# Performance work log

Hardware: AMD Instinct MI355X
Metric: run time of the kernel (lower is better)

## Reference

```python
import jax, jax.numpy as jnp
import numpy as np

B, S, D, H = 1, 2048, 768, 12
WIN = 128            # window_size
HALF = WIN // 2      # 64
WN = WIN + 1         # each position attends to [i-64, i+64] inclusive -> 129 keys
DH = D // H


def setup_inputs() -> dict:
    key = jax.random.key(0)
    ks = jax.random.split(key, 8)
    scale = 0.02
    return {
        "query": jax.random.normal(ks[0], (B, S, D), dtype=jnp.float32),
        "key":   jax.random.normal(ks[1], (B, S, D), dtype=jnp.float32),
        "value": jax.random.normal(ks[2], (B, S, D), dtype=jnp.float32),
        "Wq": jax.random.normal(ks[3], (D, D), dtype=jnp.float32) * scale,
        "bq": jnp.zeros((D,), dtype=jnp.float32),
        "Wk": jax.random.normal(ks[4], (D, D), dtype=jnp.float32) * scale,
        "bk": jnp.zeros((D,), dtype=jnp.float32),
        "Wv": jax.random.normal(ks[5], (D, D), dtype=jnp.float32) * scale,
        "bv": jnp.zeros((D,), dtype=jnp.float32),
        "Wo": jax.random.normal(ks[6], (D, D), dtype=jnp.float32) * scale,
        "bo": jnp.zeros((D,), dtype=jnp.float32),
    }


def reference(query, key, value, Wq, bq, Wk, bk, Wv, bv, Wo, bo):
    b, s, d = query.shape
    # Linear projections, split heads: [B,S,H,DH]
    q = (query @ Wq + bq).reshape(b, s, H, DH)
    k = (key   @ Wk + bk).reshape(b, s, H, DH)
    v = (value @ Wv + bv).reshape(b, s, H, DH)

    # Window gather indices: pos[i, j] = i - HALF + j, j in [0, WN)
    pos = jnp.arange(s)[:, None] + (jnp.arange(WN)[None, :] - HALF)  # [S, WN]
    valid = (pos >= 0) & (pos < s)                                   # [S, WN]
    idx = jnp.clip(pos, 0, s - 1)

    kw = k[:, idx]  # [B, S, WN, H, DH]
    vw = v[:, idx]  # [B, S, WN, H, DH]

    scores = jnp.einsum('bshd,bswhd->bhsw', q, kw) / np.sqrt(DH)     # [B,H,S,WN]
    scores = jnp.where(valid[None, None, :, :], scores, -jnp.inf)
    attn = jax.nn.softmax(scores, axis=-1)

    ctx = jnp.einsum('bhsw,bswhd->bshd', attn, vw).reshape(b, s, d)  # [B,S,D]
    return ctx @ Wo + bo
```

## Files before the change

### kernel.cpp

```cpp
#include <hip/hip_runtime.h>
#include <math.h>

#define S_LEN 2048
#define DM 768
#define NHEAD 12
#define DHEAD 64
#define HALF_W 64

typedef _Float16 half8 __attribute__((ext_vector_type(8)));
typedef _Float16 half4_t __attribute__((ext_vector_type(4)));
typedef float floatx4 __attribute__((ext_vector_type(4)));

typedef const __attribute__((address_space(1))) unsigned int* gas_ptr;
typedef __attribute__((address_space(3))) unsigned int* las_ptr;
__device__ __forceinline__ void gld_lds16(const void* g, void* l) {
  __builtin_amdgcn_global_load_lds((gas_ptr)g, (las_ptr)l, 16, 0, 0);
}

__global__ __launch_bounds__(256)
void prep_kernel(const float* __restrict__ Wq, const float* __restrict__ Wk,
                 const float* __restrict__ Wv, const float* __restrict__ Wo,
                 _Float16* __restrict__ Tq, _Float16* __restrict__ Tk,
                 _Float16* __restrict__ Tv, _Float16* __restrict__ To,
                 const float* __restrict__ qs, const float* __restrict__ ks,
                 const float* __restrict__ vs, _Float16* __restrict__ Aq,
                 _Float16* __restrict__ Ak, _Float16* __restrict__ Av) {
  __shared__ float t[64][65];
  int b = blockIdx.x;
  if (b < 576) {
    int z = b / 144, rem = b % 144;
    const float* W = z == 0 ? Wq : z == 1 ? Wk : z == 2 ? Wv : Wo;
    _Float16* T = z == 0 ? Tq : z == 1 ? Tk : z == 2 ? Tv : To;
    int n0 = (rem % 12) * 64, k0 = (rem / 12) * 64;
    int tx = threadIdx.x & 15, ty = threadIdx.x >> 4;
#pragma unroll
    for (int i = 0; i < 4; ++i) {
      int row = ty + i * 16;
      float4 v = *(const float4*)(W + (size_t)(k0 + row) * DM + n0 + tx * 4);
      t[row][tx * 4 + 0] = v.x; t[row][tx * 4 + 1] = v.y;
      t[row][tx * 4 + 2] = v.z; t[row][tx * 4 + 3] = v.w;
    }
    __syncthreads();
#pragma unroll
    for (int i = 0; i < 4; ++i) {
      int nn = ty + i * 16, kk = tx * 4;
      half4_t h = {(_Float16)t[kk + 0][nn], (_Float16)t[kk + 1][nn],
                   (_Float16)t[kk + 2][nn], (_Float16)t[kk + 3][nn]};
      *(half4_t*)(T + (size_t)(n0 + nn) * DM + k0 + kk) = h;
    }
  } else {
    int i = b - 576;
    int z = i / 1536;
    const float* s = z == 0 ? qs : z == 1 ? ks : vs;
    _Float16* d = z == 0 ? Aq : z == 1 ? Ak : Av;
    int idx = (i % 1536) * 256 + threadIdx.x;
    float4 v = ((const float4*)s)[idx];
    half4_t h = {(_Float16)v.x, (_Float16)v.y, (_Float16)v.z, (_Float16)v.w};
    ((half4_t*)d)[idx] = h;
  }
}

#define GBM 128
#define GBN 128
#define GBK 64

__global__ __launch_bounds__(256, 2)
void gemm_f16_kernel(const _Float16* __restrict__ A0, const _Float16* __restrict__ A1,
                     const _Float16* __restrict__ A2, const _Float16* __restrict__ W0,
                     const _Float16* __restrict__ W1, const _Float16* __restrict__ W2,
                     const float* __restrict__ b0, const float* __restrict__ b1,
                     const float* __restrict__ b2, _Float16* __restrict__ H0,
                     _Float16* __restrict__ H1, _Float16* __restrict__ Vt,
                     float* __restrict__ Cf, int fp32_out) {
  __shared__ __align__(16) _Float16 As[GBM * GBK];
  __shared__ __align__(16) _Float16 Bs[GBN * GBK];
  const int z = blockIdx.z;
  const _Float16* A = z == 0 ? A0 : z == 1 ? A1 : A2;
  const _Float16* Wt = z == 0 ? W0 : z == 1 ? W1 : W2;
  const float* bias = z == 0 ? b0 : z == 1 ? b1 : b2;

  const int tid = threadIdx.x;
  const int lane = tid & 63;
  const int w = tid >> 6;
  const int lr = lane & 15;
  const int lq = lane >> 4;
  const int wm = w >> 1, wn = w & 1;
  const int m0 = blockIdx.y * GBM;
  const int n0 = blockIdx.x * GBN;
  const int wb = tid & 192;

  floatx4 acc[4][4] = {};

  for (int k0 = 0; k0 < DM; k0 += GBK) {
    __syncthreads();
#pragma unroll
    for (int i = 0; i < 4; ++i) {
      int c = i * 256 + tid;
      int m = c >> 3, j = c & 7;
      int jg = j ^ (m & 7);
      gld_lds16(A + (size_t)(m0 + m) * DM + k0 + jg * 8, &As[(i * 256 + wb) * 8]);
    }
#pragma unroll
    for (int i = 0; i < 4; ++i) {
      int c = i * 256 + tid;
      int n = c >> 3, j = c & 7;
      int jg = j ^ (n & 7);
      gld_lds16(Wt + (size_t)(n0 + n) * DM + k0 + jg * 8, &Bs[(i * 256 + wb) * 8]);
    }
    __syncthreads();

#pragma unroll
    for (int kh = 0; kh < 2; ++kh) {
      half8 af[4], bf[4];
#pragma unroll
      for (int mt = 0; mt < 4; ++mt) {
        int m = wm * 64 + mt * 16 + lr;
        int j = (kh * 4 + lq) ^ (m & 7);
        af[mt] = *(const half8*)&As[m * GBK + j * 8];
      }
#pragma unroll
      for (int nt = 0; nt < 4; ++nt) {
        int n = wn * 64 + nt * 16 + lr;
        int j = (kh * 4 + lq) ^ (n & 7);
        bf[nt] = *(const half8*)&Bs[n * GBK + j * 8];
      }
#pragma unroll
      for (int mt = 0; mt < 4; ++mt)
#pragma unroll
        for (int nt = 0; nt < 4; ++nt)
          acc[mt][nt] = __builtin_amdgcn_mfma_f32_16x16x32_f16(af[mt], bf[nt], acc[mt][nt], 0, 0, 0);
    }
  }

#pragma unroll
  for (int mt = 0; mt < 4; ++mt) {
    int row0 = m0 + wm * 64 + mt * 16 + lq * 4;
#pragma unroll
    for (int nt = 0; nt < 4; ++nt) {
      int col = n0 + wn * 64 + nt * 16 + lr;
      float bv = bias[col];
      if (fp32_out) {
#pragma unroll
        for (int rr = 0; rr < 4; ++rr)
          Cf[(size_t)(row0 + rr) * DM + col] = acc[mt][nt][rr] + bv;
      } else if (z == 2) {
        half4_t o = {(_Float16)(acc[mt][nt][0] + bv), (_Float16)(acc[mt][nt][1] + bv),
                     (_Float16)(acc[mt][nt][2] + bv), (_Float16)(acc[mt][nt][3] + bv)};
        *(half4_t*)(Vt + (size_t)col * S_LEN + row0) = o;
      } else {
        _Float16* H = z == 0 ? H0 : H1;
#pragma unroll
        for (int rr = 0; rr < 4; ++rr)
          H[(size_t)(row0 + rr) * DM + col] = (_Float16)(acc[mt][nt][rr] + bv);
      }
    }
  }
}

#define ATQ 32
#define AR 160
#define VTC 24

__global__ __launch_bounds__(256, 2)
void swattn_mfma_kernel(const _Float16* __restrict__ qh, const _Float16* __restrict__ kh,
                        const _Float16* __restrict__ vt, _Float16* __restrict__ ctx) {
  __shared__ __align__(16) _Float16 Qs[ATQ * DHEAD];
  __shared__ __align__(16) _Float16 Ks[AR * DHEAD];
  __shared__ __align__(16) _Float16 Vs[DHEAD * VTC * 8];
  __shared__ float Sbuf[ATQ][161];
  __shared__ __align__(16) _Float16 Pbuf[ATQ][168];

  const int tid = threadIdx.x;
  const int lane = tid & 63, w = tid >> 6;
  const int lr = lane & 15, lq = lane >> 4;
  const int s0 = blockIdx.x * ATQ;
  const int h = blockIdx.y;
  const int wb = tid & 192;

  {
    int r = tid >> 3, j = tid & 7;
    int jg = j ^ (r & 7);
    gld_lds16(qh + (size_t)(s0 + r) * DM + h * DHEAD + jg * 8, &Qs[wb * 8]);
  }
#pragma unroll
  for (int i = 0; i < 5; ++i) {
    int c = i * 256 + tid;
    int r = c >> 3, j = c & 7;
    int jg = j ^ (r & 7);
    int pos = s0 - HALF_W + r;
    pos = pos < 0 ? 0 : (pos > S_LEN - 1 ? S_LEN - 1 : pos);
    gld_lds16(kh + (size_t)pos * DM + h * DHEAD + jg * 8, &Ks[(i * 256 + wb) * 8]);
  }
#pragma unroll
  for (int i = 0; i < 6; ++i) {
    int c = i * 256 + tid;
    int r = c / VTC, j = c % VTC;
    int jg = j ^ (r & 7);
    int cb = s0 - HALF_W + jg * 8;
    cb = cb < 0 ? 0 : (cb > S_LEN - 8 ? S_LEN - 8 : cb);
    gld_lds16(vt + (size_t)(h * DHEAD + r) * S_LEN + cb, &Vs[(i * 256 + wb) * 8]);
  }
  __syncthreads();

  {
    const int qt = w >> 1;
    const int ptb = (w & 1) * 5;
    half8 aq[2];
#pragma unroll
    for (int k2 = 0; k2 < 2; ++k2) {
      int r = qt * 16 + lr, j = (k2 * 4 + lq) ^ (r & 7);
      aq[k2] = *(const half8*)&Qs[r * DHEAD + j * 8];
    }
#pragma unroll
    for (int i = 0; i < 5; ++i) {
      int pt = ptb + i;
      floatx4 acc = {};
#pragma unroll
      for (int k2 = 0; k2 < 2; ++k2) {
        int r = pt * 16 + lr, j = (k2 * 4 + lq) ^ (r & 7);
        half8 bk = *(const half8*)&Ks[r * DHEAD + j * 8];
        acc = __builtin_amdgcn_mfma_f32_16x16x32_f16(aq[k2], bk, acc, 0, 0, 0);
      }
#pragma unroll
      for (int rr = 0; rr < 4; ++rr)
        Sbuf[qt * 16 + lq * 4 + rr][pt * 16 + lr] = acc[rr] * 0.125f;
    }
  }
  __syncthreads();

#pragma unroll
  for (int i = 0; i < 8; ++i) {
    int q = w * 8 + i;
    int p0 = lane, p1 = 64 + lane, p2 = 128 + lane;
    int g0 = s0 - HALF_W + p0, g1 = s0 + lane, g2 = s0 + HALF_W + lane;
    bool ok0 = (p0 >= q) && (g0 >= 0);
    bool ok1 = (g1 < S_LEN);
    bool ok2 = (lane <= q) && (g2 < S_LEN);
    float sv0 = ok0 ? Sbuf[q][p0] : -1e30f;
    float sv1 = ok1 ? Sbuf[q][p1] : -1e30f;
    float sv2 = ok2 ? Sbuf[q][p2] : -1e30f;
    float mx = fmaxf(sv0, fmaxf(sv1, sv2));
#pragma unroll
    for (int off = 32; off > 0; off >>= 1) mx = fmaxf(mx, __shfl_xor(mx, off, 64));
    float e0 = __expf(sv0 - mx), e1 = __expf(sv1 - mx), e2 = __expf(sv2 - mx);
    float sum = e0 + e1 + e2;
#pragma unroll
    for (int off = 32; off > 0; off >>= 1) sum += __shfl_xor(sum, off, 64);
    float inv = 1.f / sum;
    Pbuf[q][p0] = (_Float16)(e0 * inv);
    Pbuf[q][p1] = (_Float16)(e1 * inv);
    if (lane < 32) Pbuf[q][p2] = (_Float16)(e2 * inv);
  }
  __syncthreads();

  {
    const int qt = w >> 1;
    const int dt0 = (w & 1) * 2;
    floatx4 a0 = {}, a1 = {};
#pragma unroll
    for (int ks = 0; ks < 5; ++ks) {
      half8 ap = *(const half8*)&Pbuf[qt * 16 + lr][ks * 32 + lq * 8];
      int r0 = dt0 * 16 + lr, r1 = (dt0 + 1) * 16 + lr;
      int j0 = (ks * 4 + lq) ^ (r0 & 7), j1 = (ks * 4 + lq) ^ (r1 & 7);
      half8 bv0 = *(const half8*)&Vs[(r0 * VTC + j0) * 8];
      half8 bv1 = *(const half8*)&Vs[(r1 * VTC + j1) * 8];
      a0 = __builtin_amdgcn_mfma_f32_16x16x32_f16(ap, bv0, a0, 0, 0, 0);
      a1 = __builtin_amdgcn_mfma_f32_16x16x32_f16(ap, bv1, a1, 0, 0, 0);
    }
#pragma unroll
    for (int rr = 0; rr < 4; ++rr) {
      size_t row = (size_t)(s0 + qt * 16 + lq * 4 + rr) * DM + h * DHEAD;
      ctx[row + dt0 * 16 + lr] = (_Float16)a0[rr];
      ctx[row + (dt0 + 1) * 16 + lr] = (_Float16)a1[rr];
    }
  }
}

extern "C" void kernel_launch(void* const* d_in, const int* in_sizes, int n_in,
                              void* d_out, int out_size, void* d_ws, size_t ws_size,
                              hipStream_t stream) {
  const float* query = (const float*)d_in[0];
  const float* key   = (const float*)d_in[1];
  const float* value = (const float*)d_in[2];
  const float* Wq = (const float*)d_in[3];
  const float* bq = (const float*)d_in[4];
  const float* Wk = (const float*)d_in[5];
  const float* bk = (const float*)d_in[6];
  const float* Wv = (const float*)d_in[7];
  const float* bv = (const float*)d_in[8];
  const float* Wo = (const float*)d_in[9];
  const float* bo = (const float*)d_in[10];
  float* out = (float*)d_out;

  const size_t nel = (size_t)S_LEN * DM;
  const size_t wel = (size_t)DM * DM;
  _Float16* Aq = (_Float16*)d_ws;
  _Float16* Ak = Aq + nel;
  _Float16* Av = Ak + nel;
  _Float16* Wtq = Av + nel;
  _Float16* Wtk = Wtq + wel;
  _Float16* Wtv = Wtk + wel;
  _Float16* Wto = Wtv + wel;
  _Float16* qh = Wto + wel;
  _Float16* khb = qh + nel;
  _Float16* Vtg = khb + nel;
  _Float16* ctxh = Aq;

  prep_kernel<<<dim3(576 + 4608), 256, 0, stream>>>(
      Wq, Wk, Wv, Wo, Wtq, Wtk, Wtv, Wto, query, key, value, Aq, Ak, Av);
  gemm_f16_kernel<<<dim3(DM / GBN, S_LEN / GBM, 3), 256, 0, stream>>>(
      Aq, Ak, Av, Wtq, Wtk, Wtv, bq, bk, bv, qh, khb, Vtg, nullptr, 0);
  swattn_mfma_kernel<<<dim3(S_LEN / ATQ, NHEAD), 256, 0, stream>>>(qh, khb, Vtg, ctxh);
  gemm_f16_kernel<<<dim3(DM / GBN, S_LEN / GBM, 1), 256, 0, stream>>>(
      ctxh, ctxh, ctxh, Wto, Wto, Wto, bo, bo, bo, nullptr, nullptr, nullptr, out, 1);
}
```

Before: 144.9 us.

## Fuse all stages into one persistent cooperative kernel with grid syncs

Replaces the four separate launches (weight and input conversion, QKV GEMM, windowed attention, output GEMM) with one persistent cooperative kernel. Its blocks loop over work units per phase and are separated by grid-wide syncs. Shared memory is a union sized for the largest phase. GEMM tiles shrink from 128x128 to 128x64 to create more tiles for the persistent grid, and the V tile in LDS drops the XOR swizzle for a padded row stride. The aim is to remove launch overhead and inter-kernel gaps, at the cost of grid-sync latency, an occupancy cap of at most two blocks per CU, and the larger unified LDS footprint.

```diff
diff --git a/kernel.cpp b/kernel.cpp
--- a/kernel.cpp
+++ b/kernel.cpp
@@ -1,5 +1,8 @@
 #include <hip/hip_runtime.h>
+#include <hip/hip_cooperative_groups.h>
 #include <math.h>
+
+namespace cg = cooperative_groups;
 
 #define S_LEN 2048
 #define DM 768
@@ -17,117 +20,65 @@
   __builtin_amdgcn_global_load_lds((gas_ptr)g, (las_ptr)l, 16, 0, 0);
 }
 
-__global__ __launch_bounds__(256)
-void prep_kernel(const float* __restrict__ Wq, const float* __restrict__ Wk,
-                 const float* __restrict__ Wv, const float* __restrict__ Wo,
-                 _Float16* __restrict__ Tq, _Float16* __restrict__ Tk,
-                 _Float16* __restrict__ Tv, _Float16* __restrict__ To,
-                 const float* __restrict__ qs, const float* __restrict__ ks,
-                 const float* __restrict__ vs, _Float16* __restrict__ Aq,
-                 _Float16* __restrict__ Ak, _Float16* __restrict__ Av) {
-  __shared__ float t[64][65];
-  int b = blockIdx.x;
-  if (b < 576) {
-    int z = b / 144, rem = b % 144;
-    const float* W = z == 0 ? Wq : z == 1 ? Wk : z == 2 ? Wv : Wo;
-    _Float16* T = z == 0 ? Tq : z == 1 ? Tk : z == 2 ? Tv : To;
-    int n0 = (rem % 12) * 64, k0 = (rem / 12) * 64;
-    int tx = threadIdx.x & 15, ty = threadIdx.x >> 4;
-#pragma unroll
-    for (int i = 0; i < 4; ++i) {
-      int row = ty + i * 16;
-      float4 v = *(const float4*)(W + (size_t)(k0 + row) * DM + n0 + tx * 4);
-      t[row][tx * 4 + 0] = v.x; t[row][tx * 4 + 1] = v.y;
-      t[row][tx * 4 + 2] = v.z; t[row][tx * 4 + 3] = v.w;
-    }
-    __syncthreads();
-#pragma unroll
-    for (int i = 0; i < 4; ++i) {
-      int nn = ty + i * 16, kk = tx * 4;
-      half4_t h = {(_Float16)t[kk + 0][nn], (_Float16)t[kk + 1][nn],
-                   (_Float16)t[kk + 2][nn], (_Float16)t[kk + 3][nn]};
-      *(half4_t*)(T + (size_t)(n0 + nn) * DM + k0 + kk) = h;
-    }
-  } else {
-    int i = b - 576;
-    int z = i / 1536;
-    const float* s = z == 0 ? qs : z == 1 ? ks : vs;
-    _Float16* d = z == 0 ? Aq : z == 1 ? Ak : Av;
-    int idx = (i % 1536) * 256 + threadIdx.x;
-    float4 v = ((const float4*)s)[idx];
-    half4_t h = {(_Float16)v.x, (_Float16)v.y, (_Float16)v.z, (_Float16)v.w};
-    ((half4_t*)d)[idx] = h;
-  }
-}
-
-#define GBM 128
-#define GBN 128
-#define GBK 64
-
-__global__ __launch_bounds__(256, 2)
-void gemm_f16_kernel(const _Float16* __restrict__ A0, const _Float16* __restrict__ A1,
-                     const _Float16* __restrict__ A2, const _Float16* __restrict__ W0,
-                     const _Float16* __restrict__ W1, const _Float16* __restrict__ W2,
-                     const float* __restrict__ b0, const float* __restrict__ b1,
-                     const float* __restrict__ b2, _Float16* __restrict__ H0,
-                     _Float16* __restrict__ H1, _Float16* __restrict__ Vt,
-                     float* __restrict__ Cf, int fp32_out) {
-  __shared__ __align__(16) _Float16 As[GBM * GBK];
-  __shared__ __align__(16) _Float16 Bs[GBN * GBK];
-  const int z = blockIdx.z;
-  const _Float16* A = z == 0 ? A0 : z == 1 ? A1 : A2;
-  const _Float16* Wt = z == 0 ? W0 : z == 1 ? W1 : W2;
-  const float* bias = z == 0 ? b0 : z == 1 ? b1 : b2;
-
+union SmemU {
+  struct { float t[64][65]; } p;
+  struct { _Float16 As[128 * 64]; _Float16 Bs[64 * 64]; } g;
+  struct {
+    _Float16 Qs[32 * 64];
+    _Float16 Ks[160 * 64];
+    _Float16 Vs[64 * 168];
+    float Sbuf[32][161];
+    _Float16 Pbuf[32][168];
+  } a;
+};
+
+__device__ __forceinline__ void gemm_tile(
+    const _Float16* __restrict__ A, const _Float16* __restrict__ Wt,
+    const float* __restrict__ bias, int m0, int n0,
+    _Float16* As, _Float16* Bs, _Float16* __restrict__ Hout,
+    _Float16* __restrict__ VtOut, float* __restrict__ Fout) {
   const int tid = threadIdx.x;
-  const int lane = tid & 63;
-  const int w = tid >> 6;
-  const int lr = lane & 15;
-  const int lq = lane >> 4;
+  const int lane = tid & 63, w = tid >> 6;
+  const int lr = lane & 15, lq = lane >> 4;
   const int wm = w >> 1, wn = w & 1;
-  const int m0 = blockIdx.y * GBM;
-  const int n0 = blockIdx.x * GBN;
   const int wb = tid & 192;
-
-  floatx4 acc[4][4] = {};
-
-  for (int k0 = 0; k0 < DM; k0 += GBK) {
+  floatx4 acc[4][2] = {};
+
+  for (int k0 = 0; k0 < DM; k0 += 64) {
     __syncthreads();
 #pragma unroll
     for (int i = 0; i < 4; ++i) {
       int c = i * 256 + tid;
-      int m = c >> 3, j = c & 7;
-      int jg = j ^ (m & 7);
+      int m = c >> 3, j = c & 7, jg = j ^ (m & 7);
       gld_lds16(A + (size_t)(m0 + m) * DM + k0 + jg * 8, &As[(i * 256 + wb) * 8]);
     }
 #pragma unroll
-    for (int i = 0; i < 4; ++i) {
+    for (int i = 0; i < 2; ++i) {
       int c = i * 256 + tid;
-      int n = c >> 3, j = c & 7;
-      int jg = j ^ (n & 7);
+      int n = c >> 3, j = c & 7, jg = j ^ (n & 7);
       gld_lds16(Wt + (size_t)(n0 + n) * DM + k0 + jg * 8, &Bs[(i * 256 + wb) * 8]);
     }
     __syncthreads();
 
 #pragma unroll
     for (int kh = 0; kh < 2; ++kh) {
-      half8 af[4], bf[4];
+      half8 af[4], bf[2];
 #pragma unroll
       for (int mt = 0; mt < 4; ++mt) {
         int m = wm * 64 + mt * 16 + lr;
         int j = (kh * 4 + lq) ^ (m & 7);
-        af[mt] = *(const half8*)&As[m * GBK + j * 8];
-      }
-#pragma unroll
-      for (int nt = 0; nt < 4; ++nt) {
-        int n = wn * 64 + nt * 16 + lr;
+        af[mt] = *(const half8*)&As[m * 64 + j * 8];
+      }
+#pragma unroll
+      for (int nt = 0; nt < 2; ++nt) {
+        int n = wn * 32 + nt * 16 + lr;
         int j = (kh * 4 + lq) ^ (n & 7);
-        bf[nt] = *(const half8*)&Bs[n * GBK + j * 8];
+        bf[nt] = *(const half8*)&Bs[n * 64 + j * 8];
       }
 #pragma unroll
       for (int mt = 0; mt < 4; ++mt)
 #pragma unroll
-        for (int nt = 0; nt < 4; ++nt)
+        for (int nt = 0; nt < 2; ++nt)
           acc[mt][nt] = __builtin_amdgcn_mfma_f32_16x16x32_f16(af[mt], bf[nt], acc[mt][nt], 0, 0, 0);
     }
   }
@@ -136,143 +87,212 @@
   for (int mt = 0; mt < 4; ++mt) {
     int row0 = m0 + wm * 64 + mt * 16 + lq * 4;
 #pragma unroll
-    for (int nt = 0; nt < 4; ++nt) {
-      int col = n0 + wn * 64 + nt * 16 + lr;
+    for (int nt = 0; nt < 2; ++nt) {
+      int col = n0 + wn * 32 + nt * 16 + lr;
       float bv = bias[col];
-      if (fp32_out) {
+      if (Fout) {
 #pragma unroll
         for (int rr = 0; rr < 4; ++rr)
-          Cf[(size_t)(row0 + rr) * DM + col] = acc[mt][nt][rr] + bv;
-      } else if (z == 2) {
+          Fout[(size_t)(row0 + rr) * DM + col] = acc[mt][nt][rr] + bv;
+      } else if (VtOut) {
         half4_t o = {(_Float16)(acc[mt][nt][0] + bv), (_Float16)(acc[mt][nt][1] + bv),
                      (_Float16)(acc[mt][nt][2] + bv), (_Float16)(acc[mt][nt][3] + bv)};
-        *(half4_t*)(Vt + (size_t)col * S_LEN + row0) = o;
+        *(half4_t*)(VtOut + (size_t)col * S_LEN + row0) = o;
       } else {
-        _Float16* H = z == 0 ? H0 : H1;
 #pragma unroll
         for (int rr = 0; rr < 4; ++rr)
-          H[(size_t)(row0 + rr) * DM + col] = (_Float16)(acc[mt][nt][rr] + bv);
+          Hout[(size_t)(row0 + rr) * DM + col] = (_Float16)(acc[mt][nt][rr] + bv);
       }
     }
   }
 }
 
-#define ATQ 32
-#define AR 160
-#define VTC 24
-
 __global__ __launch_bounds__(256, 2)
-void swattn_mfma_kernel(const _Float16* __restrict__ qh, const _Float16* __restrict__ kh,
-                        const _Float16* __restrict__ vt, _Float16* __restrict__ ctx) {
-  __shared__ __align__(16) _Float16 Qs[ATQ * DHEAD];
-  __shared__ __align__(16) _Float16 Ks[AR * DHEAD];
-  __shared__ __align__(16) _Float16 Vs[DHEAD * VTC * 8];
-  __shared__ float Sbuf[ATQ][161];
-  __shared__ __align__(16) _Float16 Pbuf[ATQ][168];
-
+void mega_kernel(const float* __restrict__ query, const float* __restrict__ key,
+                 const float* __restrict__ value, const float* __restrict__ Wq,
+                 const float* __restrict__ bq, const float* __restrict__ Wk,
+                 const float* __restrict__ bk, const float* __restrict__ Wv,
+                 const float* __restrict__ bv, const float* __restrict__ Wo,
+                 const float* __restrict__ bo, float* __restrict__ out,
+                 _Float16* __restrict__ ws) {
+  __shared__ __align__(16) SmemU sm;
   const int tid = threadIdx.x;
-  const int lane = tid & 63, w = tid >> 6;
-  const int lr = lane & 15, lq = lane >> 4;
-  const int s0 = blockIdx.x * ATQ;
-  const int h = blockIdx.y;
-  const int wb = tid & 192;
-
-  {
-    int r = tid >> 3, j = tid & 7;
-    int jg = j ^ (r & 7);
-    gld_lds16(qh + (size_t)(s0 + r) * DM + h * DHEAD + jg * 8, &Qs[wb * 8]);
-  }
-#pragma unroll
-  for (int i = 0; i < 5; ++i) {
-    int c = i * 256 + tid;
-    int r = c >> 3, j = c & 7;
-    int jg = j ^ (r & 7);
-    int pos = s0 - HALF_W + r;
-    pos = pos < 0 ? 0 : (pos > S_LEN - 1 ? S_LEN - 1 : pos);
-    gld_lds16(kh + (size_t)pos * DM + h * DHEAD + jg * 8, &Ks[(i * 256 + wb) * 8]);
-  }
-#pragma unroll
-  for (int i = 0; i < 6; ++i) {
-    int c = i * 256 + tid;
-    int r = c / VTC, j = c % VTC;
-    int jg = j ^ (r & 7);
-    int cb = s0 - HALF_W + jg * 8;
-    cb = cb < 0 ? 0 : (cb > S_LEN - 8 ? S_LEN - 8 : cb);
-    gld_lds16(vt + (size_t)(h * DHEAD + r) * S_LEN + cb, &Vs[(i * 256 + wb) * 8]);
-  }
-  __syncthreads();
-
-  {
-    const int qt = w >> 1;
-    const int ptb = (w & 1) * 5;
-    half8 aq[2];
-#pragma unroll
-    for (int k2 = 0; k2 < 2; ++k2) {
-      int r = qt * 16 + lr, j = (k2 * 4 + lq) ^ (r & 7);
-      aq[k2] = *(const half8*)&Qs[r * DHEAD + j * 8];
+  const int nblk = gridDim.x;
+  const size_t nel = (size_t)S_LEN * DM;
+  const size_t wel = (size_t)DM * DM;
+  _Float16* Aq = ws;
+  _Float16* Ak = Aq + nel;
+  _Float16* Av = Ak + nel;
+  _Float16* Wtq = Av + nel;
+  _Float16* Wtk = Wtq + wel;
+  _Float16* Wtv = Wtk + wel;
+  _Float16* Wto = Wtv + wel;
+  _Float16* qh = Wto + wel;
+  _Float16* khb = qh + nel;
+  _Float16* Vtg = khb + nel;
+  _Float16* ctxh = Aq;
+  cg::grid_group grid = cg::this_grid();
+
+  for (int u = blockIdx.x; u < 864; u += nblk) {
+    if (u < 576) {
+      __syncthreads();
+      int z = u / 144, rem = u % 144;
+      const float* W = z == 0 ? Wq : z == 1 ? Wk : z == 2 ? Wv : Wo;
+      _Float16* T = z == 0 ? Wtq : z == 1 ? Wtk : z == 2 ? Wtv : Wto;
+      int n0 = (rem % 12) * 64, k0 = (rem / 12) * 64;
+      int tx = tid & 15, ty = tid >> 4;
+#pragma unroll
+      for (int i = 0; i < 4; ++i) {
+        int row = ty + i * 16;
+        float4 v = *(const float4*)(W + (size_t)(k0 + row) * DM + n0 + tx * 4);
+        sm.p.t[row][tx * 4 + 0] = v.x; sm.p.t[row][tx * 4 + 1] = v.y;
+        sm.p.t[row][tx * 4 + 2] = v.z; sm.p.t[row][tx * 4 + 3] = v.w;
+      }
+      __syncthreads();
+#pragma unroll
+      for (int i = 0; i < 4; ++i) {
+        int nn = ty + i * 16, kk = tx * 4;
+        half4_t h = {(_Float16)sm.p.t[kk + 0][nn], (_Float16)sm.p.t[kk + 1][nn],
+                     (_Float16)sm.p.t[kk + 2][nn], (_Float16)sm.p.t[kk + 3][nn]};
+        *(half4_t*)(T + (size_t)(n0 + nn) * DM + k0 + kk) = h;
+      }
+    } else {
+      int u2 = u - 576;
+      int z = u2 / 96, part = u2 % 96;
+      const float* s = z == 0 ? query : z == 1 ? key : value;
+      _Float16* d = z == 0 ? Aq : z == 1 ? Ak : Av;
+#pragma unroll
+      for (int jj = 0; jj < 16; ++jj) {
+        int idx = part * 4096 + jj * 256 + tid;
+        float4 v = ((const float4*)s)[idx];
+        half4_t h = {(_Float16)v.x, (_Float16)v.y, (_Float16)v.z, (_Float16)v.w};
+        ((half4_t*)d)[idx] = h;
+      }
+    }
+  }
+  __threadfence(); grid.sync(); __threadfence();
+
+  for (int u = blockIdx.x; u < 576; u += nblk) {
+    int z = u / 192, rem = u % 192;
+    int m0 = (rem / 12) * 128, n0 = (rem % 12) * 64;
+    const _Float16* A = z == 0 ? Aq : z == 1 ? Ak : Av;
+    const _Float16* Wt = z == 0 ? Wtq : z == 1 ? Wtk : Wtv;
+    const float* bias = z == 0 ? bq : z == 1 ? bk : bv;
+    gemm_tile(A, Wt, bias, m0, n0, sm.g.As, sm.g.Bs,
+              z == 0 ? qh : khb, z == 2 ? Vtg : nullptr, nullptr);
+  }
+  __threadfence(); grid.sync(); __threadfence();
+
+  for (int u = blockIdx.x; u < 768; u += nblk) {
+    __syncthreads();
+    const int s0 = (u & 63) * 32;
+    const int h = u >> 6;
+    const int lane = tid & 63, w = tid >> 6;
+    const int lr = lane & 15, lq = lane >> 4;
+    const int wb = tid & 192;
+
+    {
+      int r = tid >> 3, j = tid & 7;
+      int jg = j ^ (r & 7);
+      gld_lds16(qh + (size_t)(s0 + r) * DM + h * DHEAD + jg * 8, &sm.a.Qs[wb * 8]);
     }
 #pragma unroll
     for (int i = 0; i < 5; ++i) {
-      int pt = ptb + i;
-      floatx4 acc = {};
+      int c = i * 256 + tid;
+      int r = c >> 3, j = c & 7;
+      int jg = j ^ (r & 7);
+      int pos = s0 - HALF_W + r;
+      pos = pos < 0 ? 0 : (pos > S_LEN - 1 ? S_LEN - 1 : pos);
+      gld_lds16(khb + (size_t)pos * DM + h * DHEAD + jg * 8, &sm.a.Ks[(i * 256 + wb) * 8]);
+    }
+#pragma unroll
+    for (int i = 0; i < 6; ++i) {
+      int c = i * 256 + tid;
+      if (c < 1344) {
+        int r = c / 21, j = c % 21;
+        int cb = s0 - HALF_W + j * 8;
+        cb = cb < 0 ? 0 : (cb > S_LEN - 8 ? S_LEN - 8 : cb);
+        gld_lds16(Vtg + (size_t)(h * DHEAD + r) * S_LEN + cb, &sm.a.Vs[(i * 256 + wb) * 8]);
+      }
+    }
+    __syncthreads();
+
+    {
+      const int qt = w >> 1;
+      const int ptb = (w & 1) * 5;
+      half8 aq[2];
 #pragma unroll
       for (int k2 = 0; k2 < 2; ++k2) {
-        int r = pt * 16 + lr, j = (k2 * 4 + lq) ^ (r & 7);
-        half8 bk = *(const half8*)&Ks[r * DHEAD + j * 8];
-        acc = __builtin_amdgcn_mfma_f32_16x16x32_f16(aq[k2], bk, acc, 0, 0, 0);
-      }
-#pragma unroll
-      for (int rr = 0; rr < 4; ++rr)
-        Sbuf[qt * 16 + lq * 4 + rr][pt * 16 + lr] = acc[rr] * 0.125f;
-    }
-  }
-  __syncthreads();
-
-#pragma unroll
-  for (int i = 0; i < 8; ++i) {
-    int q = w * 8 + i;
-    int p0 = lane, p1 = 64 + lane, p2 = 128 + lane;
-    int g0 = s0 - HALF_W + p0, g1 = s0 + lane, g2 = s0 + HALF_W + lane;
-    bool ok0 = (p0 >= q) && (g0 >= 0);
-    bool ok1 = (g1 < S_LEN);
-    bool ok2 = (lane <= q) && (g2 < S_LEN);
-    float sv0 = ok0 ? Sbuf[q][p0] : -1e30f;
-    float sv1 = ok1 ? Sbuf[q][p1] : -1e30f;
-    float sv2 = ok2 ? Sbuf[q][p2] : -1e30f;
-    float mx = fmaxf(sv0, fmaxf(sv1, sv2));
-#pragma unroll
-    for (int off = 32; off > 0; off >>= 1) mx = fmaxf(mx, __shfl_xor(mx, off, 64));
-    float e0 = __expf(sv0 - mx), e1 = __expf(sv1 - mx), e2 = __expf(sv2 - mx);
-    float sum = e0 + e1 + e2;
-#pragma unroll
-    for (int off = 32; off > 0; off >>= 1) sum += __shfl_xor(sum, off, 64);
-    float inv = 1.f / sum;
-    Pbuf[q][p0] = (_Float16)(e0 * inv);
-    Pbuf[q][p1] = (_Float16)(e1 * inv);
-    if (lane < 32) Pbuf[q][p2] = (_Float16)(e2 * inv);
-  }
-  __syncthreads();
-
-  {
-    const int qt = w >> 1;
-    const int dt0 = (w & 1) * 2;
-    floatx4 a0 = {}, a1 = {};
-#pragma unroll
-    for (int ks = 0; ks < 5; ++ks) {
-      half8 ap = *(const half8*)&Pbuf[qt * 16 + lr][ks * 32 + lq * 8];
-      int r0 = dt0 * 16 + lr, r1 = (dt0 + 1) * 16 + lr;
-      int j0 = (ks * 4 + lq) ^ (r0 & 7), j1 = (ks * 4 + lq) ^ (r1 & 7);
-      half8 bv0 = *(const half8*)&Vs[(r0 * VTC + j0) * 8];
-      half8 bv1 = *(const half8*)&Vs[(r1 * VTC + j1) * 8];
-      a0 = __builtin_amdgcn_mfma_f32_16x16x32_f16(ap, bv0, a0, 0, 0, 0);
-      a1 = __builtin_amdgcn_mfma_f32_16x16x32_f16(ap, bv1, a1, 0, 0, 0);
-    }
-#pragma unroll
-    for (int rr = 0; rr < 4; ++rr) {
-      size_t row = (size_t)(s0 + qt * 16 + lq * 4 + rr) * DM + h * DHEAD;
-      ctx[row + dt0 * 16 + lr] = (_Float16)a0[rr];
-      ctx[row + (dt0 + 1) * 16 + lr] = (_Float16)a1[rr];
-    }
+        int r = qt * 16 + lr, j = (k2 * 4 + lq) ^ (r & 7);
+        aq[k2] = *(const half8*)&sm.a.Qs[r * DHEAD + j * 8];
+      }
+#pragma unroll
+      for (int i = 0; i < 5; ++i) {
+        int pt = ptb + i;
+        floatx4 acc = {};
+#pragma unroll
+        for (int k2 = 0; k2 < 2; ++k2) {
+          int r = pt * 16 + lr, j = (k2 * 4 + lq) ^ (r & 7);
+          half8 bk2 = *(const half8*)&sm.a.Ks[r * DHEAD + j * 8];
+          acc = __builtin_amdgcn_mfma_f32_16x16x32_f16(aq[k2], bk2, acc, 0, 0, 0);
+        }
+#pragma unroll
+        for (int rr = 0; rr < 4; ++rr)
+          sm.a.Sbuf[qt * 16 + lq * 4 + rr][pt * 16 + lr] = acc[rr] * 0.125f;
+      }
+    }
+    __syncthreads();
+
+#pragma unroll
+    for (int i = 0; i < 8; ++i) {
+      int q = w * 8 + i;
+      int p0 = lane, p1 = 64 + lane, p2 = 128 + lane;
+      int g0 = s0 - HALF_W + p0, g1 = s0 + lane, g2 = s0 + HALF_W + lane;
+      bool ok0 = (p0 >= q) && (g0 >= 0);
+      bool ok1 = (g1 < S_LEN);
+      bool ok2 = (lane <= q) && (g2 < S_LEN);
+      float sv0 = ok0 ? sm.a.Sbuf[q][p0] : -1e30f;
+      float sv1 = ok1 ? sm.a.Sbuf[q][p1] : -1e30f;
+      float sv2 = ok2 ? sm.a.Sbuf[q][p2] : -1e30f;
+      float mx = fmaxf(sv0, fmaxf(sv1, sv2));
+#pragma unroll
+      for (int off = 32; off > 0; off >>= 1) mx = fmaxf(mx, __shfl_xor(mx, off, 64));
+      float e0 = __expf(sv0 - mx), e1 = __expf(sv1 - mx), e2 = __expf(sv2 - mx);
+      float sum = e0 + e1 + e2;
+#pragma unroll
+      for (int off = 32; off > 0; off >>= 1) sum += __shfl_xor(sum, off, 64);
+      float inv = 1.f / sum;
+      sm.a.Pbuf[q][p0] = (_Float16)(e0 * inv);
+      sm.a.Pbuf[q][p1] = (_Float16)(e1 * inv);
+      if (lane < 32) sm.a.Pbuf[q][p2] = (_Float16)(e2 * inv);
+    }
+    __syncthreads();
+
+    {
+      const int qt = w >> 1;
+      const int dt0 = (w & 1) * 2;
+      floatx4 a0 = {}, a1 = {};
+#pragma unroll
+      for (int ks = 0; ks < 5; ++ks) {
+        half8 ap = *(const half8*)&sm.a.Pbuf[qt * 16 + lr][ks * 32 + lq * 8];
+        half8 bv0 = *(const half8*)&sm.a.Vs[(dt0 * 16 + lr) * 168 + ks * 32 + lq * 8];
+        half8 bv1 = *(const half8*)&sm.a.Vs[((dt0 + 1) * 16 + lr) * 168 + ks * 32 + lq * 8];
+        a0 = __builtin_amdgcn_mfma_f32_16x16x32_f16(ap, bv0, a0, 0, 0, 0);
+        a1 = __builtin_amdgcn_mfma_f32_16x16x32_f16(ap, bv1, a1, 0, 0, 0);
+      }
+#pragma unroll
+      for (int rr = 0; rr < 4; ++rr) {
+        size_t row = (size_t)(s0 + qt * 16 + lq * 4 + rr) * DM + h * DHEAD;
+        ctxh[row + dt0 * 16 + lr] = (_Float16)a0[rr];
+        ctxh[row + (dt0 + 1) * 16 + lr] = (_Float16)a1[rr];
+      }
+    }
+  }
+  __threadfence(); grid.sync(); __threadfence();
+
+  for (int u = blockIdx.x; u < 192; u += nblk) {
+    int m0 = (u / 12) * 128, n0 = (u % 12) * 64;
+    gemm_tile(ctxh, Wto, bo, m0, n0, sm.g.As, sm.g.Bs, nullptr, nullptr, out);
   }
 }
 
@@ -291,26 +311,15 @@
   const float* Wo = (const float*)d_in[9];
   const float* bo = (const float*)d_in[10];
   float* out = (float*)d_out;
-
-  const size_t nel = (size_t)S_LEN * DM;
-  const size_t wel = (size_t)DM * DM;
-  _Float16* Aq = (_Float16*)d_ws;
-  _Float16* Ak = Aq + nel;
-  _Float16* Av = Ak + nel;
-  _Float16* Wtq = Av + nel;
-  _Float16* Wtk = Wtq + wel;
-  _Float16* Wtv = Wtk + wel;
-  _Float16* Wto = Wtv + wel;
-  _Float16* qh = Wto + wel;
-  _Float16* khb = qh + nel;
-  _Float16* Vtg = khb + nel;
-  _Float16* ctxh = Aq;
-
-  prep_kernel<<<dim3(576 + 4608), 256, 0, stream>>>(
-      Wq, Wk, Wv, Wo, Wtq, Wtk, Wtv, Wto, query, key, value, Aq, Ak, Av);
-  gemm_f16_kernel<<<dim3(DM / GBN, S_LEN / GBM, 3), 256, 0, stream>>>(
-      Aq, Ak, Av, Wtq, Wtk, Wtv, bq, bk, bv, qh, khb, Vtg, nullptr, 0);
-  swattn_mfma_kernel<<<dim3(S_LEN / ATQ, NHEAD), 256, 0, stream>>>(qh, khb, Vtg, ctxh);
-  gemm_f16_kernel<<<dim3(DM / GBN, S_LEN / GBM, 1), 256, 0, stream>>>(
-      ctxh, ctxh, ctxh, Wto, Wto, Wto, bo, bo, bo, nullptr, nullptr, nullptr, out, 1);
+  _Float16* ws = (_Float16*)d_ws;
+
+  int maxb = 0;
+  hipOccupancyMaxActiveBlocksPerMultiprocessor(&maxb, (const void*)mega_kernel, 256, 0);
+  if (maxb < 1) maxb = 1;
+  int grid = 256 * maxb;
+  if (grid > 512) grid = 512;
+
+  void* args[] = {&query, &key, &value, &Wq, &bq, &Wk, &bk,
+                  &Wv, &bv, &Wo, &bo, &out, &ws};
+  hipLaunchCooperativeKernel((void*)mega_kernel, dim3(grid), dim3(256), args, 0, stream);
 }
```

Result: slower. 399.9 us (+176.0%).
